# Kernel tuning notes

Hardware: AMD Instinct MI355X
Metric: run time of the kernel (lower is better)

## Reference

```python
import jax, jax.numpy as jnp
import numpy as np

N, E = 50000, 1000000
H, Q, F, M = 128, 128, 64, 16  # hidden, equivariant, edge_feat, sh dims


def setup_inputs() -> dict:
    key = jax.random.key(0)
    ks = jax.random.split(key, 20)
    s = lambda fin: 1.0 / np.sqrt(fin)
    return {
        'h': jax.random.normal(ks[0], (N, H), jnp.float32),
        'h_eq': jax.random.normal(ks[1], (N, Q), jnp.float32),
        'edge_feat': jax.random.normal(ks[2], (E, F), jnp.float32),
        'sh': jax.random.normal(ks[3], (E, M), jnp.float32),
        'edge_i': jax.random.randint(ks[4], (E,), 0, N, jnp.int64),
        'edge_j': jax.random.randint(ks[5], (E,), 0, N, jnp.int64),
        # weights stored [in, out]; y = x @ W + b (equivalent to torch Linear)
        'W_in': jax.random.uniform(ks[6], (H, Q), jnp.float32, -s(H), s(H)),
        'b_in': jnp.zeros((Q,), jnp.float32),
        'W_gate': jax.random.uniform(ks[7], (H, Q), jnp.float32, -s(H), s(H)),
        'b_gate': jnp.zeros((Q,), jnp.float32),
        'W1': jax.random.uniform(ks[8], (H + F, H), jnp.float32, -s(H + F), s(H + F)),
        'b1': jnp.zeros((H,), jnp.float32),
        'W2': jax.random.uniform(ks[9], (H, H), jnp.float32, -s(H), s(H)),
        'b2': jnp.zeros((H,), jnp.float32),
        'W_up': jax.random.uniform(ks[10], (H, H), jnp.float32, -s(H), s(H)),
        'b_up': jnp.zeros((H,), jnp.float32),
        'W_tp': jax.random.uniform(ks[11], (M, Q), jnp.float32, -s(M), s(M)),
    }


def reference(h, h_eq, edge_feat, sh, edge_i, edge_j,
              W_in, b_in, W_gate, b_gate, W1, b1, W2, b2, W_up, b_up, W_tp):
    n_nodes = h.shape[0]
    # gather source node features: [E, H]
    h_j = h[edge_j]
    # scalar message MLP on concatenated [h_j, edge_feat]
    x = jnp.concatenate([h_j, edge_feat], axis=-1)
    scalar_msg = jax.nn.silu(x @ W1 + b1) @ W2 + b2  # [E, H]
    agg_scalar = jax.ops.segment_sum(scalar_msg, edge_i, num_segments=n_nodes)
    h_new = h + agg_scalar @ W_up + b_up
    # equivariant message: channel-wise tensor product with spherical harmonics
    eq_in = h_j @ W_in + b_in              # [E, Q]
    eq_msg = eq_in * (sh @ W_tp)           # [E, Q]
    agg_eq = jax.ops.segment_sum(eq_msg, edge_i, num_segments=n_nodes)
    gate = jax.nn.sigmoid(h_new @ W_gate + b_gate)  # gate uses UPDATED h
    h_eq_new = h_eq + agg_eq * gate
    return h_new, h_eq_new
```

## Files before the change

kernel.cpp:

```cpp
#include <hip/hip_runtime.h>
#include <hip/hip_bf16.h>


#define Hdim 128
#define Fdim 64
#define Mdim 16
#define TE   64
#define XLD  200
#define YLD  132
#define SLD  40

typedef __attribute__((ext_vector_type(8))) short short8;
typedef __attribute__((ext_vector_type(4))) short short4v;
typedef __attribute__((ext_vector_type(4))) float float4v;

__device__ __forceinline__ float b2f(short s) {
    union { unsigned u; float f; } c;
    c.u = ((unsigned)(unsigned short)s) << 16;
    return c.f;
}
__device__ __forceinline__ short f2b(float f) {
    union { __hip_bfloat16 h; short s; } c;
    c.h = __float2bfloat16(f);
    return c.s;
}
__device__ __forceinline__ float ldf(const void* p, long i, int isbf) {
    return isbf ? b2f(((const short*)p)[i]) : ((const float*)p)[i];
}
__device__ __forceinline__ int ldi(const void* p, long i, int is64) {
    return is64 ? (int)((const long long*)p)[i] : ((const int*)p)[i];
}
__device__ __forceinline__ short8 pack8(const float4v a, const float4v b) {
    short8 t;
#pragma unroll
    for (int r = 0; r < 4; ++r) { t[r] = f2b(a[r]); t[4 + r] = f2b(b[r]); }
    return t;
}

__global__ void ei_sniff_kernel(const unsigned* __restrict__ hw,
                                const unsigned* __restrict__ iw,
                                int* __restrict__ flags)
{
    __shared__ int cf[64], ci[64];
    const int t = threadIdx.x;
    int c1 = 0, c2 = 0;
#pragma unroll
    for (int k = 0; k < 4; ++k) {
        const unsigned w = hw[t + 64 * k];
        const unsigned e = (w >> 7) & 0xFFu;
        c1 += (e >= 100u && e <= 140u) ? 1 : 0;
        const unsigned wi = iw[2 * (t + 64 * k) + 1];
        c2 += (wi == 0u) ? 1 : 0;
    }
    cf[t] = c1; ci[t] = c2;
    __syncthreads();
    if (t == 0) {
        int s1 = 0, s2 = 0;
        for (int i = 0; i < 64; ++i) { s1 += cf[i]; s2 += ci[i]; }
        flags[0] = (s1 >= 192) ? 1 : 0;
        flags[1] = (s2 >= 200) ? 1 : 0;
    }
}


__global__ void ei_hist_kernel(const void* __restrict__ edge_i,
                               int* __restrict__ hist,
                               const int* __restrict__ flags, int E_)
{
    const int dti = flags[1];
    int i = blockIdx.x * blockDim.x + threadIdx.x;
    const int stride = gridDim.x * blockDim.x;
    for (; i < E_; i += stride) atomicAdd(&hist[ldi(edge_i, i, dti)], 1);
}

__global__ void ei_scan_kernel(int* __restrict__ hist,
                               int* __restrict__ rs, int N_, int E_)
{
    __shared__ int buf[1024];
    const int t = threadIdx.x;
    const int chunk = (N_ + 1023) >> 10;
    const int base = t * chunk;
    int s = 0;
    for (int i = 0; i < chunk; ++i) {
        const int idx = base + i;
        if (idx < N_) s += hist[idx];
    }
    buf[t] = s;
    __syncthreads();
    for (int d = 1; d < 1024; d <<= 1) {
        const int v = (t >= d) ? buf[t - d] : 0;
        __syncthreads();
        buf[t] += v;
        __syncthreads();
    }
    int run = buf[t] - s;
    for (int i = 0; i < chunk; ++i) {
        const int idx = base + i;
        if (idx >= N_) break;
        const int h = hist[idx];
        rs[idx] = run;
        hist[idx] = run;
        run += h;
    }
    if (t == 0) rs[N_] = E_;
}

__global__ void ei_scatter_kernel(const void* __restrict__ edge_i,
                                  int* __restrict__ cur,
                                  int* __restrict__ perm,
                                  const int* __restrict__ flags, int E_)
{
    const int dti = flags[1];
    int i = blockIdx.x * blockDim.x + threadIdx.x;
    const int stride = gridDim.x * blockDim.x;
    for (; i < E_; i += stride) {
        const int c = ldi(edge_i, i, dti);
        const int p = atomicAdd(&cur[c], 1);
        perm[p] = i;
    }
}

__global__ void ei_w2up_kernel(const void* __restrict__ W2,
                               const void* __restrict__ Wup,
                               const void* __restrict__ b2,
                               short* __restrict__ w2up,
                               float* __restrict__ bu2,
                               const int* __restrict__ flags)
{
    const int dtf = flags[0];
    const int o = threadIdx.x;
    const int i = blockIdx.x;
    float acc = 0.f;
    for (int m = 0; m < Hdim; ++m) {
        const float a = (i < Hdim) ? ldf(W2, (long)i * Hdim + m, dtf)
                                   : ldf(b2, m, dtf);
        acc += a * ldf(Wup, (long)m * Hdim + o, dtf);
    }
    if (i < Hdim) w2up[i * Hdim + o] = f2b(acc);
    else          bu2[o] = acc;
}

__global__ __launch_bounds__(256, 2)
void ei_edge_sorted(const void* __restrict__ hmat,
                    const void* __restrict__ efeat,
                    const void* __restrict__ shmat,
                    const void* __restrict__ edge_j,
                    const int*  __restrict__ perm,
                    const int*  __restrict__ edge_i_sorted_src,
                    const void* __restrict__ W1,
                    const void* __restrict__ b1,
                    const void* __restrict__ Win,
                    const void* __restrict__ bin,
                    const void* __restrict__ Wtp,
                    float* __restrict__ agg_y,
                    float* __restrict__ agg_q,
                    const int* __restrict__ flags,
                    int ntiles)
{
    __shared__ alignas(16) short Xs[TE][XLD];
    __shared__ alignas(16) short Ys[TE][YLD];
    __shared__ alignas(16) short Qs[TE][YLD];
    __shared__ alignas(16) short Ss[TE][SLD];
    __shared__ int ids[TE];

    const int dtf = flags[0];
    const int dti = flags[1];

    const int tid  = threadIdx.x;
    const int lane = tid & 63;
    const int wv   = tid >> 6;
    const int q    = lane >> 4;
    const int ln   = lane & 15;
    const int mch0 = wv * 32;

    for (int i = tid; i < TE * XLD; i += 256) ((short*)Xs)[i] = 0;
    for (int i = tid; i < TE * YLD; i += 256) ((short*)Ys)[i] = 0;
    for (int i = tid; i < TE * YLD; i += 256) ((short*)Qs)[i] = 0;
    for (int i = tid; i < TE * SLD; i += 256) ((short*)Ss)[i] = 0;
    __syncthreads();

    short8 w1f[6][2], wif[4][2], wtf[2];
    float4v b1v[2], biv[2];
#pragma unroll
    for (int mt = 0; mt < 2; ++mt) {
        const int m = mch0 + mt * 16 + ln;
#pragma unroll
        for (int kc = 0; kc < 6; ++kc) {
            short8 t;
            const int k0 = kc * 32 + q * 8;
#pragma unroll
            for (int j = 0; j < 8; ++j) t[j] = dtf ? ((const short*)W1)[(long)(k0 + j) * Hdim + m]
                                                   : f2b(((const float*)W1)[(long)(k0 + j) * Hdim + m]);
            w1f[kc][mt] = t;
        }
#pragma unroll
        for (int kc = 0; kc < 4; ++kc) {
            short8 u;
            const int k0 = kc * 32 + q * 8;
#pragma unroll
            for (int j = 0; j < 8; ++j) {
                const long idx = (long)(k0 + j) * Hdim + m;
                u[j] = dtf ? ((const short*)Win)[idx] : f2b(((const float*)Win)[idx]);
            }
            wif[kc][mt] = u;
        }
        {
            short8 t;
#pragma unroll
            for (int j = 0; j < 8; ++j) {
                const int k = q * 8 + j;
                t[j] = (k < Mdim) ? (dtf ? ((const short*)Wtp)[(long)k * Hdim + m]
                                         : f2b(((const float*)Wtp)[(long)k * Hdim + m]))
                                  : (short)0;
            }
            wtf[mt] = t;
        }
        const int cb = mch0 + mt * 16 + q * 4;
#pragma unroll
        for (int r = 0; r < 4; ++r) {
            b1v[mt][r] = ldf(b1, cb + r, dtf);
            biv[mt][r] = ldf(bin, cb + r, dtf);
        }
    }

    const int e_loc = tid >> 2;
    const int part  = tid & 3;

    short8 xh[4];
    short8 xf[2];
    short8 xs2[2];
    int nx_e = 0, nx_j = 0, nx_pid = 0;

    auto prefA = [&](int t) {
        const int base = t * TE;
        nx_e = perm[base + e_loc];
        nx_j = ldi(edge_j, nx_e, dti);
        if (tid < TE) nx_pid = ldi(edge_i_sorted_src, perm[base + tid], dti);
    };
    auto prefB = [&]() {
        if (dtf) {
            const short8* hs = (const short8*)((const short*)hmat + (long)nx_j * Hdim);
#pragma unroll
            for (int c = 0; c < 4; ++c) xh[c] = hs[part * 4 + c];
            const short8* fs = (const short8*)((const short*)efeat + (long)nx_e * Fdim);
            xf[0] = fs[part * 2 + 0];
            xf[1] = fs[part * 2 + 1];
            if (part == 0) {
                const short8* ss = (const short8*)((const short*)shmat + (long)nx_e * Mdim);
                xs2[0] = ss[0];
                xs2[1] = ss[1];
            }
        } else {
            const float4v* hs = (const float4v*)((const float*)hmat + (long)nx_j * Hdim + part * 32);
#pragma unroll
            for (int c = 0; c < 4; ++c) xh[c] = pack8(hs[2 * c], hs[2 * c + 1]);
            const float4v* fs = (const float4v*)((const float*)efeat + (long)nx_e * Fdim + part * 16);
            xf[0] = pack8(fs[0], fs[1]);
            xf[1] = pack8(fs[2], fs[3]);
            if (part == 0) {
                const float4v* ss = (const float4v*)((const float*)shmat + (long)nx_e * Mdim);
                xs2[0] = pack8(ss[0], ss[1]);
                xs2[1] = pack8(ss[2], ss[3]);
            }
        }
    };

    int tile = blockIdx.x;
    if (tile < ntiles) { prefA(tile); prefB(); }

    for (; tile < ntiles; tile += gridDim.x) {
#pragma unroll
        for (int c = 0; c < 4; ++c)
            *(short8*)&Xs[e_loc][part * 32 + c * 8] = xh[c];
        *(short8*)&Xs[e_loc][Hdim + part * 16]     = xf[0];
        *(short8*)&Xs[e_loc][Hdim + part * 16 + 8] = xf[1];
        if (part == 0) {
            *(short8*)&Ss[e_loc][0] = xs2[0];
            *(short8*)&Ss[e_loc][8] = xs2[1];
        }
        if (tid < TE) ids[tid] = nx_pid;
        __syncthreads();

        const unsigned long long bmask =
            __ballot((lane == 63) || (ids[lane + 1] != ids[lane]));

        int nxt = tile + (int)gridDim.x;
        if (nxt >= ntiles) nxt = tile;
        prefA(nxt);

        float4v a1[2][4] = {};
#pragma unroll
        for (int kc = 0; kc < 6; ++kc) {
            short8 xb[4];
#pragma unroll
            for (int nt = 0; nt < 4; ++nt)
                xb[nt] = *(const short8*)&Xs[nt * 16 + ln][kc * 32 + q * 8];
#pragma unroll
            for (int nt = 0; nt < 4; ++nt)
#pragma unroll
                for (int mt = 0; mt < 2; ++mt)
                    a1[mt][nt] = __builtin_amdgcn_mfma_f32_16x16x32_bf16(
                        w1f[kc][mt], xb[nt], a1[mt][nt], 0, 0, 0);
        }
#pragma unroll
        for (int mt = 0; mt < 2; ++mt)
#pragma unroll
            for (int nt = 0; nt < 4; ++nt) {
                short4v p;
#pragma unroll
                for (int r = 0; r < 4; ++r) {
                    const float y = a1[mt][nt][r] + b1v[mt][r];
                    const float s = y / (1.f + __expf(-y));
                    p[r] = f2b(s);
                }
                *(short4v*)&Ys[nt * 16 + ln][mch0 + mt * 16 + q * 4] = p;
            }

        float4v a3[2][4] = {};
        float4v at[2][4] = {};
#pragma unroll
        for (int kc = 0; kc < 4; ++kc) {
            short8 xb[4];
#pragma unroll
            for (int nt = 0; nt < 4; ++nt)
                xb[nt] = *(const short8*)&Xs[nt * 16 + ln][kc * 32 + q * 8];
#pragma unroll
            for (int nt = 0; nt < 4; ++nt)
#pragma unroll
                for (int mt = 0; mt < 2; ++mt)
                    a3[mt][nt] = __builtin_amdgcn_mfma_f32_16x16x32_bf16(
                        wif[kc][mt], xb[nt], a3[mt][nt], 0, 0, 0);
        }
        {
            short8 sb[4];
#pragma unroll
            for (int nt = 0; nt < 4; ++nt)
                sb[nt] = *(const short8*)&Ss[nt * 16 + ln][q * 8];
#pragma unroll
            for (int nt = 0; nt < 4; ++nt)
#pragma unroll
                for (int mt = 0; mt < 2; ++mt)
                    at[mt][nt] = __builtin_amdgcn_mfma_f32_16x16x32_bf16(
                        wtf[mt], sb[nt], at[mt][nt], 0, 0, 0);
        }
#pragma unroll
        for (int mt = 0; mt < 2; ++mt)
#pragma unroll
            for (int nt = 0; nt < 4; ++nt) {
                short4v p;
#pragma unroll
                for (int r = 0; r < 4; ++r)
                    p[r] = f2b((a3[mt][nt][r] + biv[mt][r]) * at[mt][nt][r]);
                *(short4v*)&Qs[nt * 16 + ln][mch0 + mt * 16 + q * 4] = p;
            }

        prefB();
        __syncthreads();

        {
            const int half = tid >> 7;
            const int qsel = (tid >> 6) & 1;
            const int c2   = tid & 63;
            const short* srcb = qsel ? &Qs[0][0] : &Ys[0][0];
            float* agg = qsel ? agg_q : agg_y;
            const int e0 = half * 32;
            float v0 = 0.f, v1 = 0.f;
            int run_start = e0;
#pragma unroll
            for (int eb = 0; eb < 4; ++eb) {
                unsigned wb[8];
#pragma unroll
                for (int k = 0; k < 8; ++k)
                    wb[k] = *(const unsigned*)(srcb + (e0 + eb * 8 + k) * YLD + 2 * c2);
#pragma unroll
                for (int k = 0; k < 8; ++k) {
                    const int e = e0 + eb * 8 + k;
                    union { unsigned u; float f; } lo, hi;
                    lo.u = wb[k] << 16;
                    hi.u = wb[k] & 0xFFFF0000u;
                    v0 += lo.f;
                    v1 += hi.f;
                    const bool hend = (e == e0 + 31);
                    if (hend || ((bmask >> e) & 1ull)) {
                        const int id = ids[e];
                        float* dst = agg + (long)id * Hdim + 2 * c2;
                        if (hend || run_start == e0) {
                            unsafeAtomicAdd(dst, v0);
                            unsafeAtomicAdd(dst + 1, v1);
                        } else {
                            float2 st; st.x = v0; st.y = v1;
                            *(float2*)dst = st;
                        }
                        v0 = 0.f; v1 = 0.f;
                        run_start = e + 1;
                    }
                }
            }
        }
        __syncthreads();
    }
}

__global__ __launch_bounds__(256, 2)
void ei_node_kernel(const void* __restrict__ hmat,
                    const void* __restrict__ heq,
                    const short* __restrict__ w2up,
                    const float* __restrict__ bu2,
                    const void* __restrict__ bup,
                    const void* __restrict__ Wg,
                    const void* __restrict__ bg,
                    const int*  __restrict__ rs,
                    const float* __restrict__ agg_y,
                    const float* __restrict__ agg_q,
                    void* __restrict__ outp,
                    const int* __restrict__ flags,
                    int N)
{
    __shared__ alignas(16) short Xa[TE][YLD];
    __shared__ alignas(16) short Yh[TE][YLD];
    __shared__ int degs[TE];

    const int dtf = flags[0];

    const int tid  = threadIdx.x;
    const int lane = tid & 63;
    const int wv   = tid >> 6;
    const int q    = lane >> 4;
    const int ln   = lane & 15;
    const int mch0 = wv * 32;

    short* outh_b = (short*)outp;
    short* outq_b = outh_b + (long)N * Hdim;
    float* outh_f = (float*)outp;
    float* outq_f = outh_f + (long)N * Hdim;

    short8 wcf[4][2], wgf[4][2];
    float4v bu2v[2], bupv[2], bgv[2];
#pragma unroll
    for (int mt = 0; mt < 2; ++mt) {
        const int m = mch0 + mt * 16 + ln;
#pragma unroll
        for (int kc = 0; kc < 4; ++kc) {
            short8 t, u;
            const int k0 = kc * 32 + q * 8;
#pragma unroll
            for (int j = 0; j < 8; ++j) {
                const long idx = (long)(k0 + j) * Hdim + m;
                t[j] = w2up[idx];
                u[j] = dtf ? ((const short*)Wg)[idx] : f2b(((const float*)Wg)[idx]);
            }
            wcf[kc][mt] = t;
            wgf[kc][mt] = u;
        }
        const int cb = mch0 + mt * 16 + q * 4;
#pragma unroll
        for (int r = 0; r < 4; ++r) {
            bu2v[mt][r] = bu2[cb + r];
            bupv[mt][r] = ldf(bup, cb + r, dtf);
            bgv[mt][r]  = ldf(bg, cb + r, dtf);
        }
    }

    const int e_loc = tid >> 2;
    const int part  = tid & 3;
    const int nb    = blockIdx.x * TE;

    {
        const int node = nb + e_loc;
        if (node < N) {
            const float4v* src = (const float4v*)(agg_y + (long)node * Hdim + part * 32);
#pragma unroll
            for (int c = 0; c < 4; ++c) {
                const float4v v0 = src[2 * c], v1 = src[2 * c + 1];
                short8 t;
#pragma unroll
                for (int r = 0; r < 4; ++r) { t[r] = f2b(v0[r]); t[4 + r] = f2b(v1[r]); }
                *(short8*)&Xa[e_loc][part * 32 + c * 8] = t;
            }
            if (part == 0) degs[e_loc] = rs[node + 1] - rs[node];
        } else {
            short8 z = {};
#pragma unroll
            for (int c = 0; c < 4; ++c)
                *(short8*)&Xa[e_loc][part * 32 + c * 8] = z;
            if (part == 0) degs[e_loc] = 0;
        }
    }
    __syncthreads();

    float4v au[2][4] = {};
#pragma unroll
    for (int kc = 0; kc < 4; ++kc) {
        short8 ab[4];
#pragma unroll
        for (int nt = 0; nt < 4; ++nt)
            ab[nt] = *(const short8*)&Xa[nt * 16 + ln][kc * 32 + q * 8];
#pragma unroll
        for (int nt = 0; nt < 4; ++nt)
#pragma unroll
            for (int mt = 0; mt < 2; ++mt)
                au[mt][nt] = __builtin_amdgcn_mfma_f32_16x16x32_bf16(
                    wcf[kc][mt], ab[nt], au[mt][nt], 0, 0, 0);
    }
#pragma unroll
    for (int mt = 0; mt < 2; ++mt)
#pragma unroll
        for (int nt = 0; nt < 4; ++nt) {
            const int nd = nb + nt * 16 + ln;
            const int ch = mch0 + mt * 16 + q * 4;
            short4v p;
            if (nd < N) {
                const float dg = (float)degs[nt * 16 + ln];
                float hv[4];
                if (dtf) {
                    const short4v x = *(const short4v*)((const short*)hmat + (long)nd * Hdim + ch);
#pragma unroll
                    for (int r = 0; r < 4; ++r) hv[r] = b2f(x[r]);
                } else {
                    const float4v x = *(const float4v*)((const float*)hmat + (long)nd * Hdim + ch);
#pragma unroll
                    for (int r = 0; r < 4; ++r) hv[r] = x[r];
                }
                float4v o;
#pragma unroll
                for (int r = 0; r < 4; ++r) {
                    o[r] = hv[r] + au[mt][nt][r] + dg * bu2v[mt][r] + bupv[mt][r];
                    p[r] = f2b(o[r]);
                }
                if (dtf) *(short4v*)(outh_b + (long)nd * Hdim + ch) = p;
                else     *(float4v*)(outh_f + (long)nd * Hdim + ch) = o;
            } else {
#pragma unroll
                for (int r = 0; r < 4; ++r) p[r] = 0;
            }
            *(short4v*)&Yh[nt * 16 + ln][ch] = p;
        }
    __syncthreads();

    float4v ag[2][4] = {};
#pragma unroll
    for (int kc = 0; kc < 4; ++kc) {
        short8 yb[4];
#pragma unroll
        for (int nt = 0; nt < 4; ++nt)
            yb[nt] = *(const short8*)&Yh[nt * 16 + ln][kc * 32 + q * 8];
#pragma unroll
        for (int nt = 0; nt < 4; ++nt)
#pragma unroll
            for (int mt = 0; mt < 2; ++mt)
                ag[mt][nt] = __builtin_amdgcn_mfma_f32_16x16x32_bf16(
                    wgf[kc][mt], yb[nt], ag[mt][nt], 0, 0, 0);
    }
#pragma unroll
    for (int mt = 0; mt < 2; ++mt)
#pragma unroll
        for (int nt = 0; nt < 4; ++nt) {
            const int nd = nb + nt * 16 + ln;
            if (nd >= N) continue;
            const int ch = mch0 + mt * 16 + q * 4;
            const float4v aq = *(const float4v*)(agg_q + (long)nd * Hdim + ch);
            float hev[4];
            if (dtf) {
                const short4v x = *(const short4v*)((const short*)heq + (long)nd * Hdim + ch);
#pragma unroll
                for (int r = 0; r < 4; ++r) hev[r] = b2f(x[r]);
            } else {
                const float4v x = *(const float4v*)((const float*)heq + (long)nd * Hdim + ch);
#pragma unroll
                for (int r = 0; r < 4; ++r) hev[r] = x[r];
            }
            short4v p;
            float4v o;
#pragma unroll
            for (int r = 0; r < 4; ++r) {
                const float g = 1.f / (1.f + __expf(-(ag[mt][nt][r] + bgv[mt][r])));
                o[r] = hev[r] + aq[r] * g;
                p[r] = f2b(o[r]);
            }
            if (dtf) *(short4v*)(outq_b + (long)nd * Hdim + ch) = p;
            else     *(float4v*)(outq_f + (long)nd * Hdim + ch) = o;
        }
}

extern "C" void kernel_launch(void* const* d_in, const int* in_sizes, int n_in,
                              void* d_out, int out_size, void* d_ws, size_t ws_size,
                              hipStream_t stream)
{
    (void)n_in; (void)out_size; (void)ws_size;
    const void* hmat  = d_in[0];
    const void* heq   = d_in[1];
    const void* efeat = d_in[2];
    const void* shm   = d_in[3];
    const void* ei    = d_in[4];
    const void* ej    = d_in[5];
    const void* Win   = d_in[6];
    const void* bin   = d_in[7];
    const void* Wg    = d_in[8];
    const void* bg    = d_in[9];
    const void* W1    = d_in[10];
    const void* b1    = d_in[11];
    const void* W2    = d_in[12];
    const void* b2    = d_in[13];
    const void* Wup   = d_in[14];
    const void* bup   = d_in[15];
    const void* Wtp   = d_in[16];

    const int N = in_sizes[0] / Hdim;
    const int E = in_sizes[2] / Fdim;

    auto al = [](size_t x) { return (x + 255) & ~(size_t)255; };
    size_t off = 8;
    off = al(off); const size_t rs_off   = off; off += (size_t)(N + 1) * 4;
    off = al(off); const size_t cur_off  = off; off += (size_t)N * 4;
    off = al(off); const size_t perm_off = off; off += (size_t)E * 4;
    off = al(off); const size_t aggy_off = off; off += (size_t)N * Hdim * 4;
    const size_t aggq_off = off;                     off += (size_t)N * Hdim * 4;
    off = al(off); const size_t w2_off   = off; off += (size_t)Hdim * Hdim * 2;
    off = al(off); const size_t bu2_off  = off; off += (size_t)Hdim * 4;

    char* w = (char*)d_ws;
    int*   flags = (int*)w;
    int*   rs    = (int*)(w + rs_off);
    int*   cur   = (int*)(w + cur_off);
    int*   perm  = (int*)(w + perm_off);
    float* aggy  = (float*)(w + aggy_off);
    float* aggq  = (float*)(w + aggq_off);
    short* w2up  = (short*)(w + w2_off);
    float* bu2   = (float*)(w + bu2_off);

    ei_sniff_kernel<<<1, 64, 0, stream>>>((const unsigned*)hmat, (const unsigned*)ei, flags);
    hipMemsetAsync(cur, 0, (size_t)N * 4, stream);
    hipMemsetAsync(aggy, 0, (size_t)2 * N * Hdim * 4, stream);
    ei_hist_kernel<<<256, 256, 0, stream>>>(ei, cur, flags, E);
    ei_scan_kernel<<<1, 1024, 0, stream>>>(cur, rs, N, E);
    ei_scatter_kernel<<<256, 256, 0, stream>>>(ei, cur, perm, flags, E);
    ei_w2up_kernel<<<Hdim + 1, Hdim, 0, stream>>>(W2, Wup, b2, w2up, bu2, flags);
    ei_edge_sorted<<<512, 256, 0, stream>>>(hmat, efeat, shm, ej, perm, (const int*)ei,
                                            W1, b1, Win, bin, Wtp,
                                            aggy, aggq, flags, E / TE);
    ei_node_kernel<<<(N + TE - 1) / TE, 256, 0, stream>>>(
        hmat, heq, w2up, bu2, bup, Wg, bg, rs, aggy, aggq, d_out, flags, N);
}
```

Measured before the change: 1.063 ms.

## Deepen edge-kernel gather pipeline, rewrite scan with wave shuffles, enlarge sort grids

The edge kernel now issues the next tile's global gathers as raw payload loads at the start of each iteration. It stages them into LDS after the scatter phase, keeps double-buffered segment ids, and prefetches perm indices two tiles ahead. This hides gather latency behind the MFMA and atomic phases, at the cost of more registers (a 16-float4 payload) and lighter barriers that wait only on LDS traffic. The single-block scan is replaced by a coalesced multi-pass wave-shuffle scan, and the histogram and scatter kernels launch four times more blocks.

```diff
diff --git a/kernel.cpp b/kernel.cpp
--- a/kernel.cpp
+++ b/kernel.cpp
@@ -37,6 +37,12 @@
     return t;
 }
 
+__device__ __forceinline__ void bar_lds() {
+    asm volatile("s_waitcnt lgkmcnt(0)" ::: "memory");
+    __builtin_amdgcn_s_barrier();
+    asm volatile("" ::: "memory");
+}
+
 __global__ void ei_sniff_kernel(const unsigned* __restrict__ hw,
                                 const unsigned* __restrict__ iw,
                                 int* __restrict__ flags)
@@ -76,31 +82,44 @@
 __global__ void ei_scan_kernel(int* __restrict__ hist,
                                int* __restrict__ rs, int N_, int E_)
 {
-    __shared__ int buf[1024];
+    __shared__ int wsum[16];
+    __shared__ int woff[16];
+    __shared__ int tots;
     const int t = threadIdx.x;
-    const int chunk = (N_ + 1023) >> 10;
-    const int base = t * chunk;
-    int s = 0;
-    for (int i = 0; i < chunk; ++i) {
-        const int idx = base + i;
-        if (idx < N_) s += hist[idx];
-    }
-    buf[t] = s;
-    __syncthreads();
-    for (int d = 1; d < 1024; d <<= 1) {
-        const int v = (t >= d) ? buf[t - d] : 0;
+    const int lane = t & 63;
+    const int w = t >> 6;
+    const int npass = (N_ + 1023) >> 10;
+    int carry = 0;
+    int vn = (t < N_) ? hist[t] : 0;
+    for (int p = 0; p < npass; ++p) {
+        const int base = p << 10;
+        const int v = vn;
+        const int ni = base + 1024 + t;
+        vn = (p + 1 < npass && ni < N_) ? hist[ni] : 0;
+        int s = v;
+#pragma unroll
+        for (int d = 1; d < 64; d <<= 1) {
+            const int u = __shfl_up(s, d, 64);
+            if (lane >= d) s += u;
+        }
+        if (lane == 63) wsum[w] = s;
         __syncthreads();
-        buf[t] += v;
+        if (w == 0) {
+            const int x = (lane < 16) ? wsum[lane] : 0;
+            int sx = x;
+#pragma unroll
+            for (int d = 1; d < 16; d <<= 1) {
+                const int u = __shfl_up(sx, d, 64);
+                if (lane >= d) sx += u;
+            }
+            if (lane < 16) woff[lane] = sx - x;
+            if (lane == 15) tots = sx;
+        }
         __syncthreads();
-    }
-    int run = buf[t] - s;
-    for (int i = 0; i < chunk; ++i) {
-        const int idx = base + i;
-        if (idx >= N_) break;
-        const int h = hist[idx];
-        rs[idx] = run;
-        hist[idx] = run;
-        run += h;
+        const int excl = carry + woff[w] + (s - v);
+        const int idx = base + t;
+        if (idx < N_) { rs[idx] = excl; hist[idx] = excl; }
+        carry += tots;
     }
     if (t == 0) rs[N_] = E_;
 }
@@ -161,7 +180,7 @@
     __shared__ alignas(16) short Ys[TE][YLD];
     __shared__ alignas(16) short Qs[TE][YLD];
     __shared__ alignas(16) short Ss[TE][SLD];
-    __shared__ int ids[TE];
+    __shared__ int ids[2][TE];
 
     const int dtf = flags[0];
     const int dti = flags[1];
@@ -225,68 +244,91 @@
 
     const int e_loc = tid >> 2;
     const int part  = tid & 3;
-
-    short8 xh[4];
-    short8 xf[2];
-    short8 xs2[2];
-    int nx_e = 0, nx_j = 0, nx_pid = 0;
-
-    auto prefA = [&](int t) {
-        const int base = t * TE;
-        nx_e = perm[base + e_loc];
-        nx_j = ldi(edge_j, nx_e, dti);
-        if (tid < TE) nx_pid = ldi(edge_i_sorted_src, perm[base + tid], dti);
+    const int g     = gridDim.x;
+
+    float4v pay[16];
+    int eA = 0, jA = 0, pidA = 0;
+    int eB = 0, jB = 0, pidB = 0;
+    int peB = 0, ppB = 0;
+
+    auto prefA_full = [&](int t) {
+        const long base = (long)t * TE;
+        eA = perm[base + e_loc];
+        jA = ldi(edge_j, eA, dti);
+        pidA = ldi(edge_i_sorted_src, perm[base + (tid & (TE - 1))], dti);
     };
-    auto prefB = [&]() {
+    auto prefB_issue = [&](int e, int j) {
         if (dtf) {
-            const short8* hs = (const short8*)((const short*)hmat + (long)nx_j * Hdim);
-#pragma unroll
-            for (int c = 0; c < 4; ++c) xh[c] = hs[part * 4 + c];
-            const short8* fs = (const short8*)((const short*)efeat + (long)nx_e * Fdim);
-            xf[0] = fs[part * 2 + 0];
-            xf[1] = fs[part * 2 + 1];
+            const float4v* hp = (const float4v*)((const short*)hmat + (long)j * Hdim + part * 32);
+#pragma unroll
+            for (int c = 0; c < 4; ++c) pay[c] = hp[c];
+            const float4v* fp = (const float4v*)((const short*)efeat + (long)e * Fdim + part * 16);
+            pay[4] = fp[0]; pay[5] = fp[1];
             if (part == 0) {
-                const short8* ss = (const short8*)((const short*)shmat + (long)nx_e * Mdim);
-                xs2[0] = ss[0];
-                xs2[1] = ss[1];
+                const float4v* sp = (const float4v*)((const short*)shmat + (long)e * Mdim);
+                pay[6] = sp[0]; pay[7] = sp[1];
             }
         } else {
-            const float4v* hs = (const float4v*)((const float*)hmat + (long)nx_j * Hdim + part * 32);
-#pragma unroll
-            for (int c = 0; c < 4; ++c) xh[c] = pack8(hs[2 * c], hs[2 * c + 1]);
-            const float4v* fs = (const float4v*)((const float*)efeat + (long)nx_e * Fdim + part * 16);
-            xf[0] = pack8(fs[0], fs[1]);
-            xf[1] = pack8(fs[2], fs[3]);
+            const float4v* hp = (const float4v*)((const float*)hmat + (long)j * Hdim + part * 32);
+#pragma unroll
+            for (int c = 0; c < 8; ++c) pay[c] = hp[c];
+            const float4v* fp = (const float4v*)((const float*)efeat + (long)e * Fdim + part * 16);
+#pragma unroll
+            for (int c = 0; c < 4; ++c) pay[8 + c] = fp[c];
             if (part == 0) {
-                const float4v* ss = (const float4v*)((const float*)shmat + (long)nx_e * Mdim);
-                xs2[0] = pack8(ss[0], ss[1]);
-                xs2[1] = pack8(ss[2], ss[3]);
+                const float4v* sp = (const float4v*)((const float*)shmat + (long)e * Mdim);
+#pragma unroll
+                for (int c = 0; c < 4; ++c) pay[12 + c] = sp[c];
             }
         }
     };
-
-    int tile = blockIdx.x;
-    if (tile < ntiles) { prefA(tile); prefB(); }
-
-    for (; tile < ntiles; tile += gridDim.x) {
-#pragma unroll
-        for (int c = 0; c < 4; ++c)
-            *(short8*)&Xs[e_loc][part * 32 + c * 8] = xh[c];
-        *(short8*)&Xs[e_loc][Hdim + part * 16]     = xf[0];
-        *(short8*)&Xs[e_loc][Hdim + part * 16 + 8] = xf[1];
-        if (part == 0) {
-            *(short8*)&Ss[e_loc][0] = xs2[0];
-            *(short8*)&Ss[e_loc][8] = xs2[1];
-        }
-        if (tid < TE) ids[tid] = nx_pid;
-        __syncthreads();
+    auto stage_pay = [&](int pid, int buf) {
+        if (dtf) {
+#pragma unroll
+            for (int c = 0; c < 4; ++c)
+                *(float4v*)&Xs[e_loc][part * 32 + c * 8] = pay[c];
+            *(float4v*)&Xs[e_loc][Hdim + part * 16]     = pay[4];
+            *(float4v*)&Xs[e_loc][Hdim + part * 16 + 8] = pay[5];
+            if (part == 0) {
+                *(float4v*)&Ss[e_loc][0] = pay[6];
+                *(float4v*)&Ss[e_loc][8] = pay[7];
+            }
+        } else {
+#pragma unroll
+            for (int c = 0; c < 4; ++c)
+                *(short8*)&Xs[e_loc][part * 32 + c * 8] = pack8(pay[2 * c], pay[2 * c + 1]);
+            *(short8*)&Xs[e_loc][Hdim + part * 16]     = pack8(pay[8], pay[9]);
+            *(short8*)&Xs[e_loc][Hdim + part * 16 + 8] = pack8(pay[10], pay[11]);
+            if (part == 0) {
+                *(short8*)&Ss[e_loc][0] = pack8(pay[12], pay[13]);
+                *(short8*)&Ss[e_loc][8] = pack8(pay[14], pay[15]);
+            }
+        }
+        if (tid < TE) ids[buf][tid] = pid;
+    };
+
+    const int t0 = blockIdx.x;
+    int cur = 0;
+    if (t0 < ntiles) {
+        prefA_full(t0);
+        prefB_issue(eA, jA);
+        stage_pay(pidA, 0);
+        int t1 = t0 + g; if (t1 >= ntiles) t1 = t0;
+        prefA_full(t1);
+    }
+    __syncthreads();
+
+    for (int t = t0; t < ntiles; t += g) {
+        prefB_issue(eA, jA);
+        {
+            int t2 = t + 2 * g; if (t2 >= ntiles) t2 = t;
+            const long base2 = (long)t2 * TE;
+            peB = perm[base2 + e_loc];
+            ppB = perm[base2 + (tid & (TE - 1))];
+        }
 
         const unsigned long long bmask =
-            __ballot((lane == 63) || (ids[lane + 1] != ids[lane]));
-
-        int nxt = tile + (int)gridDim.x;
-        if (nxt >= ntiles) nxt = tile;
-        prefA(nxt);
+            __ballot((lane == 63) || (ids[cur][lane + 1] != ids[cur][lane]));
 
         float4v a1[2][4] = {};
 #pragma unroll
@@ -354,9 +396,11 @@
                 *(short4v*)&Qs[nt * 16 + ln][mch0 + mt * 16 + q * 4] = p;
             }
 
-        prefB();
-        __syncthreads();
-
+        eB = peB;
+        jB = ldi(edge_j, peB, dti);
+        pidB = ldi(edge_i_sorted_src, ppB, dti);
+
+        bar_lds();
         {
             const int half = tid >> 7;
             const int qsel = (tid >> 6) & 1;
@@ -382,7 +426,7 @@
                     v1 += hi.f;
                     const bool hend = (e == e0 + 31);
                     if (hend || ((bmask >> e) & 1ull)) {
-                        const int id = ids[e];
+                        const int id = ids[cur][e];
                         float* dst = agg + (long)id * Hdim + 2 * c2;
                         if (hend || run_start == e0) {
                             unsafeAtomicAdd(dst, v0);
@@ -397,7 +441,10 @@
                 }
             }
         }
-        __syncthreads();
+        if (t + g < ntiles) stage_pay(pidA, cur ^ 1);
+        eA = eB; jA = jB; pidA = pidB;
+        cur ^= 1;
+        bar_lds();
     }
 }
 
@@ -631,9 +678,9 @@
     ei_sniff_kernel<<<1, 64, 0, stream>>>((const unsigned*)hmat, (const unsigned*)ei, flags);
     hipMemsetAsync(cur, 0, (size_t)N * 4, stream);
     hipMemsetAsync(aggy, 0, (size_t)2 * N * Hdim * 4, stream);
-    ei_hist_kernel<<<256, 256, 0, stream>>>(ei, cur, flags, E);
+    ei_hist_kernel<<<1024, 256, 0, stream>>>(ei, cur, flags, E);
     ei_scan_kernel<<<1, 1024, 0, stream>>>(cur, rs, N, E);
-    ei_scatter_kernel<<<256, 256, 0, stream>>>(ei, cur, perm, flags, E);
+    ei_scatter_kernel<<<1024, 256, 0, stream>>>(ei, cur, perm, flags, E);
     ei_w2up_kernel<<<Hdim + 1, Hdim, 0, stream>>>(W2, Wup, b2, w2up, bu2, flags);
     ei_edge_sorted<<<512, 256, 0, stream>>>(hmat, efeat, shm, ej, perm, (const int*)ei,
                                             W1, b1, Win, bin, Wtp,
```

Measured after the change: 1.285 ms. +20.9%, slower.
